# Performance work log

Measured on AMD Instinct MI355X. Metric: run time of the kernel, lower is better.

Reference implementation:

```python
import jax, jax.numpy as jnp
import numpy as np

GROUP_SIZE = 128


def setup_inputs() -> dict:
    key = jax.random.key(0)
    k1, k2, k3, k4, k5, k6 = jax.random.split(key, 6)
    M, K, N = 8192, 4096, 11008
    num_groups = K // GROUP_SIZE  # 32
    x = (jax.random.normal(k1, (M, K), dtype=jnp.float32)).astype(jnp.float16)
    # packed uint8 bytes, each holding two int4 nibbles (stored as int32 for harness)
    packed_weight = jax.random.randint(k2, (N, K // 2), 0, 256, dtype=jnp.int32)
    # per-group, per-output-channel scales (positive, small) and zero points
    weight_scale = (jax.random.uniform(k3, (num_groups, N), dtype=jnp.float32) * 0.02 + 0.001).astype(jnp.float16)
    weight_zero = (jax.random.normal(k4, (num_groups, N), dtype=jnp.float32) * 0.5).astype(jnp.float16)
    # positive per-input-channel smoothing factors in a moderate range
    smooth_scale = (jax.random.uniform(k5, (K,), dtype=jnp.float32) * 1.5 + 0.5).astype(jnp.float16)
    bias = (jax.random.normal(k6, (N,), dtype=jnp.float32) * 0.02).astype(jnp.float16)
    return {"x": x, "packed_weight": packed_weight, "weight_scale": weight_scale,
            "weight_zero": weight_zero, "smooth_scale": smooth_scale, "bias": bias}


def _dequant_weight(packed_weight, weight_scale, weight_zero, K):
    # unpack two INT4 values per byte: even k -> low nibble, odd k -> high nibble
    low = (packed_weight & 15) - 8          # [N, K/2] int
    high = ((packed_weight >> 4) & 15) - 8  # [N, K/2] int
    N = packed_weight.shape[0]
    w_int = jnp.stack([low, high], axis=-1).reshape(N, -1)[:, :K]  # [N, K]
    # per-group dequant: group index along K
    g = jnp.arange(K) // GROUP_SIZE          # [K]
    scale = weight_scale[g]                  # [K, N] fp16
    zp = weight_zero[g]                      # [K, N] fp16
    # (q - zp) * scale, laid out [K, N] for x @ W
    return (w_int.astype(jnp.float16).T - zp) * scale


def reference(x, packed_weight, weight_scale, weight_zero, smooth_scale, bias):
    K = x.shape[-1]
    # per-channel smoothing of activations
    xs = (x / smooth_scale).astype(jnp.float16)           # [M, K]
    w_deq = _dequant_weight(packed_weight, weight_scale, weight_zero, K)  # [K, N]
    out = jnp.dot(xs, w_deq) + bias[None, :]              # [M, N] fp16
    return out.astype(jnp.float16)
```

## Files before the change

kernel.cpp:

```cpp
#include <hip/hip_runtime.h>
#include <hip/hip_fp16.h>

typedef _Float16 f16;
typedef _Float16 f16x8 __attribute__((ext_vector_type(8)));
typedef float f32x4 __attribute__((ext_vector_type(4)));
typedef int int4v __attribute__((ext_vector_type(4)));

#define BM 128
#define BN 128
#define NBUF 3
#define BUFSZ 16384

typedef const __attribute__((address_space(1))) unsigned int* gas_ptr;
typedef __attribute__((address_space(3))) unsigned int* las_ptr;

__device__ __forceinline__ void gload_lds16(const void* g, void* l) {
    __builtin_amdgcn_global_load_lds((gas_ptr)g, (las_ptr)l, 16, 0, 0);
}

__global__ __launch_bounds__(256) void quantx_kernel(
    const float* __restrict__ x, const float* __restrict__ smooth,
    char* __restrict__ Aq, float* __restrict__ sx, f16* __restrict__ U,
    int M, int K)
{
    const int row = blockIdx.x * 4 + (threadIdx.x >> 6);
    const int lane = threadIdx.x & 63;
    if (row >= M) return;

    f32x4 xsv[16];
    float amax = 0.f;
#pragma unroll
    for (int j = 0; j < 16; ++j) {
        const int k = j * 256 + lane * 4;
        const f32x4 xv = *(const f32x4*)(x + (size_t)row * K + k);
        const f32x4 sv = *(const f32x4*)(smooth + k);
        f32x4 r;
#pragma unroll
        for (int e = 0; e < 4; ++e) {
            r[e] = xv[e] / sv[e];
            amax = fmaxf(amax, fabsf(r[e]));
        }
        xsv[j] = r;
    }
#pragma unroll
    for (int off = 1; off < 64; off <<= 1)
        amax = fmaxf(amax, __shfl_xor(amax, off));
    const float sxr = fmaxf(amax, 1e-20f) / 127.f;
    const float inv = 127.f / fmaxf(amax, 1e-20f);
    if (lane == 0) sx[row] = sxr;

    int* aq32 = (int*)(Aq + (size_t)row * K);
#pragma unroll
    for (int j = 0; j < 16; ++j) {
        unsigned int pk = 0;
        float s4 = 0.f;
#pragma unroll
        for (int e = 0; e < 4; ++e) {
            const float v = xsv[j][e];
            s4 += v;
            int qi = (int)__builtin_rintf(v * inv);
            qi = qi > 127 ? 127 : (qi < -127 ? -127 : qi);
            pk |= ((unsigned int)(qi & 255)) << (8 * e);
        }
        aq32[j * 64 + lane] = (int)pk;
#pragma unroll
        for (int off = 1; off < 32; off <<= 1)
            s4 += __shfl_xor(s4, off);
        if ((lane & 31) == 0)
            U[(size_t)row * 32 + 2 * j + (lane >> 5)] = (f16)s4;
    }
}

__global__ __launch_bounds__(256) void repackw_kernel(
    const int* __restrict__ packed, char* __restrict__ Wq, int total8)
{
    const int i = blockIdx.x * 256 + threadIdx.x;
    if (i >= total8) return;
    const int4v p0 = *(const int4v*)(packed + i * 8);
    const int4v p1 = *(const int4v*)(packed + i * 8 + 4);
    int4v o;
#pragma unroll
    for (int w = 0; w < 4; ++w) {
        const int a = (w < 2) ? p0[2 * w] : p1[2 * (w - 2)];
        const int b = (w < 2) ? p0[2 * w + 1] : p1[2 * (w - 2) + 1];
        const int l0 = ((a & 15) - 8) & 255, h0 = (((a >> 4) & 15) - 8) & 255;
        const int l1 = ((b & 15) - 8) & 255, h1 = (((b >> 4) & 15) - 8) & 255;
        o[w] = l0 | (h0 << 8) | (l1 << 16) | (h1 << 24);
    }
    *(int4v*)(Wq + (size_t)i * 16) = o;
}

__global__ __launch_bounds__(256) void vneg_kernel(
    const float* __restrict__ wscale, const float* __restrict__ wzero,
    f16* __restrict__ Vneg, int N)
{
    const int i = blockIdx.x * 256 + threadIdx.x;
    if (i >= N * 32) return;
    const int n = i >> 5;
    const int g = i & 31;
    Vneg[i] = (f16)(-wscale[(size_t)g * N + n] * wzero[(size_t)g * N + n]);
}

__global__ __launch_bounds__(256, 3) void gemm_kernel(
    const char* __restrict__ Aq,
    const char* __restrict__ Wq,
    const float* __restrict__ wscale,
    const float* __restrict__ sx,
    const f16* __restrict__ U,
    const f16* __restrict__ Vneg,
    const float* __restrict__ bias,
    float* __restrict__ C,
    int M, int N, int K)
{
    __shared__ char lds[NBUF * BUFSZ];

    const int t = threadIdx.x;
    const int lane = t & 63;
    const int wid = t >> 6;
    const int wr = wid >> 1;
    const int wc = wid & 1;
    const int fr = lane & 15;
    const int fq = lane >> 4;

    const int nbm = M / BM;
    const int nbn = N / BN;
    const int nwg = nbm * nbn;
    const int bid = (int)blockIdx.x;
    const int cpx = nwg >> 3;
    const int wg = ((nwg & 7) == 0) ? ((bid & 7) * cpx + (bid >> 3)) : bid;
    const int bm = wg % nbm;
    const int bn = wg / nbm;
    const size_t m0 = (size_t)bm * BM;
    const size_t n0 = (size_t)bn * BN;

    const int scv = (t & 7) ^ ((t >> 3) & 7);
    const int rbase = 2 * (t >> 3) + (scv >> 2);
    const int kb = (scv & 3) * 16;
    const char* gAq = Aq + (m0 + rbase) * (size_t)K + kb;
    const char* gWq = Wq + (n0 + rbase) * (size_t)K + kb;

#define STAGE_AB(sb, Tst) do { char* _d = lds + (sb) + t * 16; \
    gload_lds16(gAq + (size_t)(Tst) * 64, _d); \
    gload_lds16(gAq + (size_t)64 * K + (size_t)(Tst) * 64, _d + 4096); \
    gload_lds16(gWq + (size_t)(Tst) * 64, _d + 8192); \
    gload_lds16(gWq + (size_t)64 * K + (size_t)(Tst) * 64, _d + 12288); } while (0)

    const int aswz = ((((fr & 1) << 2) | fq) ^ ((fr >> 1) & 7)) << 4;
    const int aBase = wr * 4096 + ((fr >> 1) << 7) + aswz;
    const int bBase = 8192 + wc * 4096 + ((fr >> 1) << 7) + aswz;

#define LDA(db, m) (*(const int4v*)(lds + (db) + aBase + (m) * 1024))
#define LDB(db, n) (*(const int4v*)(lds + (db) + bBase + (n) * 1024))

    f32x4 accf[4][4];
#pragma unroll
    for (int m = 0; m < 4; ++m)
#pragma unroll
        for (int n = 0; n < 4; ++n)
            accf[m][n] = {0.f, 0.f, 0.f, 0.f};

    const int4v kz = {0, 0, 0, 0};
    const int NT = K >> 6;

    STAGE_AB(0, 0);
    STAGE_AB(BUFSZ, 1);
    float sgc[4], sgn[4];
#pragma unroll
    for (int n = 0; n < 4; ++n)
        sgc[n] = wscale[n0 + wc * 64 + n * 16 + fr];
    asm volatile("s_waitcnt vmcnt(0)" ::: "memory");
    __builtin_amdgcn_s_barrier();

#pragma unroll 1
    for (int T = 0; T < NT; ++T) {
        const int db = (T % 3) * BUFSZ;
        const int sb = ((T + 2) % 3) * BUFSZ;

        if (T + 2 < NT) STAGE_AB(sb, T + 2);
        if ((T & 1) && (T >> 1) + 1 < 32) {
#pragma unroll
            for (int n = 0; n < 4; ++n)
                sgn[n] = wscale[(size_t)((T >> 1) + 1) * N + n0 + wc * 64 + n * 16 + fr];
        }

        int4v bfr[4];
#pragma unroll
        for (int n = 0; n < 4; ++n) bfr[n] = LDB(db, n);

        __builtin_amdgcn_s_setprio(1);
#pragma unroll
        for (int m = 0; m < 4; ++m) {
            const int4v av = LDA(db, m);
#pragma unroll
            for (int n = 0; n < 4; ++n) {
                const int4v tv = __builtin_amdgcn_mfma_i32_16x16x64_i8(
                    av, bfr[n], kz, 0, 0, 0);
#pragma unroll
                for (int e = 0; e < 4; ++e)
                    accf[m][n][e] += sgc[n] * (float)tv[e];
            }
        }
        __builtin_amdgcn_s_setprio(0);

        if (T & 1) {
#pragma unroll
            for (int n = 0; n < 4; ++n) sgc[n] = sgn[n];
        }

        asm volatile("s_waitcnt vmcnt(0)" ::: "memory");
        __builtin_amdgcn_s_barrier();
    }

#pragma unroll
    for (int m = 0; m < 4; ++m) {
        const f32x4 sxv = *(const f32x4*)(sx + m0 + wr * 64 + m * 16 + fq * 4);
#pragma unroll
        for (int n = 0; n < 4; ++n)
#pragma unroll
            for (int e = 0; e < 4; ++e)
                accf[m][n][e] *= sxv[e];
    }

    {
        f16x8 uf[4], vf[4];
#pragma unroll
        for (int m = 0; m < 4; ++m)
            uf[m] = *(const f16x8*)(U + (m0 + wr * 64 + m * 16 + fr) * 32 + fq * 8);
#pragma unroll
        for (int n = 0; n < 4; ++n)
            vf[n] = *(const f16x8*)(Vneg + (n0 + wc * 64 + n * 16 + fr) * 32 + fq * 8);
#pragma unroll
        for (int m = 0; m < 4; ++m)
#pragma unroll
            for (int n = 0; n < 4; ++n)
                accf[m][n] = __builtin_amdgcn_mfma_f32_16x16x32_f16(
                    uf[m], vf[n], accf[m][n], 0, 0, 0);
    }

#pragma unroll
    for (int n = 0; n < 4; ++n) {
        const size_t gcol = n0 + wc * 64 + n * 16 + fr;
        const float bv = bias[gcol];
#pragma unroll
        for (int am = 0; am < 4; ++am) {
            const size_t grow = m0 + wr * 64 + am * 16 + fq * 4;
#pragma unroll
            for (int r = 0; r < 4; ++r)
                C[(grow + r) * N + gcol] = accf[am][n][r] + bv;
        }
    }
}

extern "C" void kernel_launch(void* const* d_in, const int* in_sizes, int n_in,
                              void* d_out, int out_size, void* d_ws, size_t ws_size,
                              hipStream_t stream) {
    const float* x      = (const float*)d_in[0];
    const int* packed   = (const int*)d_in[1];
    const float* wscale = (const float*)d_in[2];
    const float* wzero  = (const float*)d_in[3];
    const float* smooth = (const float*)d_in[4];
    const float* bias   = (const float*)d_in[5];
    float* out = (float*)d_out;

    const int K = in_sizes[4];
    const int N = in_sizes[5];
    const int M = in_sizes[0] / K;
    const size_t MK = (size_t)M * K;
    const size_t NK = (size_t)N * K;

    char* Aq  = (char*)d_ws;
    char* Wq  = Aq + MK;
    f16* U    = (f16*)(Wq + NK);
    f16* Vneg = U + (size_t)M * 32;
    float* sxp = (float*)(Vneg + (size_t)N * 32);

    quantx_kernel<<<(M + 3) / 4, 256, 0, stream>>>(x, smooth, Aq, sxp, U, M, K);
    const int total8 = (int)(NK / 16);
    repackw_kernel<<<(total8 + 255) / 256, 256, 0, stream>>>(packed, Wq, total8);
    vneg_kernel<<<(N * 32 + 255) / 256, 256, 0, stream>>>(wscale, wzero, Vneg, N);

    const int grid_gemm = (M / BM) * (N / BN);
    gemm_kernel<<<grid_gemm, 256, 0, stream>>>(
        Aq, Wq, wscale, sxp, U, Vneg, bias, out, M, N, K);
}
```

Before: 745.8 us.

## Process two K-tiles per group iteration with int accumulation across both

```diff
diff --git a/kernel.cpp b/kernel.cpp
--- a/kernel.cpp
+++ b/kernel.cpp
@@ -161,6 +161,7 @@
 
     const int4v kz = {0, 0, 0, 0};
     const int NT = K >> 6;
+    const int NG = K >> 7;
 
     STAGE_AB(0, 0);
     STAGE_AB(BUFSZ, 1);
@@ -172,37 +173,47 @@
     __builtin_amdgcn_s_barrier();
 
 #pragma unroll 1
-    for (int T = 0; T < NT; ++T) {
-        const int db = (T % 3) * BUFSZ;
-        const int sb = ((T + 2) % 3) * BUFSZ;
-
-        if (T + 2 < NT) STAGE_AB(sb, T + 2);
-        if ((T & 1) && (T >> 1) + 1 < 32) {
+    for (int g = 0; g < NG; ++g) {
+        const int T0 = 2 * g;
+        const int db0 = (T0 % 3) * BUFSZ;
+        const int db1 = ((T0 + 1) % 3) * BUFSZ;
+        const int fb  = ((T0 + 2) % 3) * BUFSZ;
+
+        if (T0 + 2 < NT) STAGE_AB(fb, T0 + 2);
+
+        int4v a0[4], a1[4], b0[4], b1[4];
+#pragma unroll
+        for (int m = 0; m < 4; ++m) { a0[m] = LDA(db0, m); a1[m] = LDA(db1, m); }
+#pragma unroll
+        for (int n = 0; n < 4; ++n) { b0[n] = LDB(db0, n); b1[n] = LDB(db1, n); }
+        asm volatile("s_waitcnt lgkmcnt(0)" ::: "memory");
+        __builtin_amdgcn_sched_barrier(0);
+        __builtin_amdgcn_s_barrier();
+
+        if (T0 + 3 < NT) STAGE_AB(db0, T0 + 3);
+
+        if (g + 1 < NG) {
 #pragma unroll
             for (int n = 0; n < 4; ++n)
-                sgn[n] = wscale[(size_t)((T >> 1) + 1) * N + n0 + wc * 64 + n * 16 + fr];
-        }
-
-        int4v bfr[4];
-#pragma unroll
-        for (int n = 0; n < 4; ++n) bfr[n] = LDB(db, n);
+                sgn[n] = wscale[(size_t)(g + 1) * N + n0 + wc * 64 + n * 16 + fr];
+        }
 
         __builtin_amdgcn_s_setprio(1);
 #pragma unroll
-        for (int m = 0; m < 4; ++m) {
-            const int4v av = LDA(db, m);
+        for (int m = 0; m < 4; ++m)
 #pragma unroll
             for (int n = 0; n < 4; ++n) {
-                const int4v tv = __builtin_amdgcn_mfma_i32_16x16x64_i8(
-                    av, bfr[n], kz, 0, 0, 0);
+                int4v tv = __builtin_amdgcn_mfma_i32_16x16x64_i8(
+                    a0[m], b0[n], kz, 0, 0, 0);
+                tv = __builtin_amdgcn_mfma_i32_16x16x64_i8(
+                    a1[m], b1[n], tv, 0, 0, 0);
 #pragma unroll
                 for (int e = 0; e < 4; ++e)
                     accf[m][n][e] += sgc[n] * (float)tv[e];
             }
-        }
         __builtin_amdgcn_s_setprio(0);
 
-        if (T & 1) {
+        if (g + 1 < NG) {
 #pragma unroll
             for (int n = 0; n < 4; ++n) sgc[n] = sgn[n];
         }
```

After: 1.768 ms. +137.1%, slower.

## Use K-tile of 128 with double buffering and chained int8 MFMA per group

Applied to the files above, without the earlier changes.

```diff
diff --git a/kernel.cpp b/kernel.cpp
--- a/kernel.cpp
+++ b/kernel.cpp
@@ -8,8 +8,6 @@
 
 #define BM 128
 #define BN 128
-#define NBUF 3
-#define BUFSZ 16384
 
 typedef const __attribute__((address_space(1))) unsigned int* gas_ptr;
 typedef __attribute__((address_space(3))) unsigned int* las_ptr;
@@ -101,7 +99,7 @@
     Vneg[i] = (f16)(-wscale[(size_t)g * N + n] * wzero[(size_t)g * N + n]);
 }
 
-__global__ __launch_bounds__(256, 3) void gemm_kernel(
+__global__ __launch_bounds__(256, 2) void gemm_kernel(
     const char* __restrict__ Aq,
     const char* __restrict__ Wq,
     const float* __restrict__ wscale,
@@ -112,7 +110,7 @@
     float* __restrict__ C,
     int M, int N, int K)
 {
-    __shared__ char lds[NBUF * BUFSZ];
+    __shared__ char lds[2 * 32768];
 
     const int t = threadIdx.x;
     const int lane = t & 63;
@@ -133,24 +131,28 @@
     const size_t m0 = (size_t)bm * BM;
     const size_t n0 = (size_t)bn * BN;
 
-    const int scv = (t & 7) ^ ((t >> 3) & 7);
-    const int rbase = 2 * (t >> 3) + (scv >> 2);
-    const int kb = (scv & 3) * 16;
-    const char* gAq = Aq + (m0 + rbase) * (size_t)K + kb;
-    const char* gWq = Wq + (n0 + rbase) * (size_t)K + kb;
-
-#define STAGE_AB(sb, Tst) do { char* _d = lds + (sb) + t * 16; \
-    gload_lds16(gAq + (size_t)(Tst) * 64, _d); \
-    gload_lds16(gAq + (size_t)64 * K + (size_t)(Tst) * 64, _d + 4096); \
-    gload_lds16(gWq + (size_t)(Tst) * 64, _d + 8192); \
-    gload_lds16(gWq + (size_t)64 * K + (size_t)(Tst) * 64, _d + 12288); } while (0)
-
-    const int aswz = ((((fr & 1) << 2) | fq) ^ ((fr >> 1) & 7)) << 4;
-    const int aBase = wr * 4096 + ((fr >> 1) << 7) + aswz;
-    const int bBase = 8192 + wc * 4096 + ((fr >> 1) << 7) + aswz;
-
-#define LDA(db, m) (*(const int4v*)(lds + (db) + aBase + (m) * 1024))
-#define LDB(db, n) (*(const int4v*)(lds + (db) + bBase + (n) * 1024))
+    const int l = lane, w = wid;
+    const int sc = (l & 7) ^ ((l >> 3) & 7);
+    const int rq = w * 8 + (l >> 3);
+    const char* gAs = Aq + (m0 + rq) * (size_t)K + sc * 16;
+    const char* gWs = Wq + (n0 + rq) * (size_t)K + sc * 16;
+
+#define STAGE_AB(sb, Tst) do { \
+    _Pragma("unroll") \
+    for (int j = 0; j < 4; ++j) { \
+        gload_lds16(gAs + (size_t)(j * 32) * K + (size_t)(Tst) * 128, \
+                    lds + (sb) + j * 4096 + t * 16); \
+        gload_lds16(gWs + (size_t)(j * 32) * K + (size_t)(Tst) * 128, \
+                    lds + (sb) + 16384 + j * 4096 + t * 16); } } while (0)
+
+    const int r7 = fr & 7;
+    const int coff0 = (fq ^ r7) << 4;
+    const int coff1 = coff0 ^ 64;
+    const int aBase = wr * 8192 + fr * 128;
+    const int bBase = 16384 + wc * 8192 + fr * 128;
+
+#define LDA(db, m, kb) (*(const int4v*)(lds + (db) + aBase + (m) * 2048 + ((kb) ? coff1 : coff0)))
+#define LDB(db, n, kb) (*(const int4v*)(lds + (db) + bBase + (n) * 2048 + ((kb) ? coff1 : coff0)))
 
     f32x4 accf[4][4];
 #pragma unroll
@@ -160,10 +162,9 @@
             accf[m][n] = {0.f, 0.f, 0.f, 0.f};
 
     const int4v kz = {0, 0, 0, 0};
-    const int NT = K >> 6;
+    const int NT = K >> 7;
 
     STAGE_AB(0, 0);
-    STAGE_AB(BUFSZ, 1);
     float sgc[4], sgn[4];
 #pragma unroll
     for (int n = 0; n < 4; ++n)
@@ -173,28 +174,32 @@
 
 #pragma unroll 1
     for (int T = 0; T < NT; ++T) {
-        const int db = (T % 3) * BUFSZ;
-        const int sb = ((T + 2) % 3) * BUFSZ;
-
-        if (T + 2 < NT) STAGE_AB(sb, T + 2);
-        if ((T & 1) && (T >> 1) + 1 < 32) {
+        const int db = (T & 1) << 15;
+        const int sb = ((T + 1) & 1) << 15;
+        const bool hn = (T + 1) < NT;
+
+        if (hn) STAGE_AB(sb, T + 1);
+        if (hn) {
 #pragma unroll
             for (int n = 0; n < 4; ++n)
-                sgn[n] = wscale[(size_t)((T >> 1) + 1) * N + n0 + wc * 64 + n * 16 + fr];
-        }
-
-        int4v bfr[4];
-#pragma unroll
-        for (int n = 0; n < 4; ++n) bfr[n] = LDB(db, n);
+                sgn[n] = wscale[(size_t)(T + 1) * N + n0 + wc * 64 + n * 16 + fr];
+        }
+
+        int4v b0[4], b1[4];
+#pragma unroll
+        for (int n = 0; n < 4; ++n) { b0[n] = LDB(db, n, 0); b1[n] = LDB(db, n, 1); }
 
         __builtin_amdgcn_s_setprio(1);
 #pragma unroll
         for (int m = 0; m < 4; ++m) {
-            const int4v av = LDA(db, m);
+            const int4v a0 = LDA(db, m, 0);
+            const int4v a1 = LDA(db, m, 1);
 #pragma unroll
             for (int n = 0; n < 4; ++n) {
-                const int4v tv = __builtin_amdgcn_mfma_i32_16x16x64_i8(
-                    av, bfr[n], kz, 0, 0, 0);
+                int4v tv = __builtin_amdgcn_mfma_i32_16x16x64_i8(
+                    a0, b0[n], kz, 0, 0, 0);
+                tv = __builtin_amdgcn_mfma_i32_16x16x64_i8(
+                    a1, b1[n], tv, 0, 0, 0);
 #pragma unroll
                 for (int e = 0; e < 4; ++e)
                     accf[m][n][e] += sgc[n] * (float)tv[e];
@@ -202,7 +207,7 @@
         }
         __builtin_amdgcn_s_setprio(0);
 
-        if (T & 1) {
+        if (hn) {
 #pragma unroll
             for (int n = 0; n < 4; ++n) sgc[n] = sgn[n];
         }
```

New measurement: 639.2 us (median of 2 runs). 1.17x faster.
